# Kernel optimization log

Measured on AMD Instinct MI355X. Metric: run time of the kernel, lower is better.

## Reference

```python
import jax, jax.numpy as jnp
import numpy as np

B = 32
IMG = 512
P = 32            # patch_size (must equal 32 so bounding_box Linear(32,4) type-checks)
G = IMG // P      # 16
N = G * G         # 256 num_patches
PD = P * P * 3    # 3072 patch_dim
D = 512           # project_dim
H = 8             # num_heads
DH = D // H
L = 4             # transformer blocks
HEAD_DIMS = [N * D, 2048, 1024, 512, 64, 32]
EPS = 1e-6


def _mk(key, shape, scale=0.02):
    return (jax.random.normal(key, shape, dtype=jnp.float32) * scale)


def setup_inputs() -> dict:
    key = jax.random.key(0)
    ks = jax.random.split(key, 32)
    inp = {"images": jax.random.normal(ks[0], (B, IMG, IMG, 3), dtype=jnp.float32)}
    # patch encoder
    inp["W_proj"] = _mk(ks[1], (PD, D))
    inp["b_proj"] = jnp.zeros((D,), jnp.float32)
    inp["pos_emb"] = _mk(ks[2], (N, D))
    # stacked transformer block params [L, ...]
    inp["ln1_g"] = jnp.ones((L, D), jnp.float32)
    inp["ln1_b"] = jnp.zeros((L, D), jnp.float32)
    inp["qkv_w"] = _mk(ks[3], (L, 3 * D, D))
    inp["qkv_b"] = jnp.zeros((L, 3 * D), jnp.float32)
    inp["attn_out_w"] = _mk(ks[4], (L, D, D))
    inp["attn_out_b"] = jnp.zeros((L, D), jnp.float32)
    inp["ln2_g"] = jnp.ones((L, D), jnp.float32)
    inp["ln2_b"] = jnp.zeros((L, D), jnp.float32)
    inp["mlp_w1"] = _mk(ks[5], (L, D, 2 * D))
    inp["mlp_b1"] = jnp.zeros((L, 2 * D), jnp.float32)
    inp["mlp_w2"] = _mk(ks[6], (L, 2 * D, D))
    inp["mlp_b2"] = jnp.zeros((L, D), jnp.float32)
    # final LN
    inp["lnf_g"] = jnp.ones((D,), jnp.float32)
    inp["lnf_b"] = jnp.zeros((D,), jnp.float32)
    # MLP head (5 layers) + bbox
    for i in range(5):
        inp[f"hW{i+1}"] = _mk(ks[7 + i], (HEAD_DIMS[i], HEAD_DIMS[i + 1]))
        inp[f"hb{i+1}"] = jnp.zeros((HEAD_DIMS[i + 1],), jnp.float32)
    inp["bbW"] = _mk(ks[20], (32, 4))
    inp["bbb"] = jnp.zeros((4,), jnp.float32)
    return inp


def _ln(x, g, b):
    m = jnp.mean(x, axis=-1, keepdims=True)
    v = jnp.mean((x - m) ** 2, axis=-1, keepdims=True)
    return (x - m) * jax.lax.rsqrt(v + EPS) * g + b


def _patches(images):
    # fused unfold: [B,IMG,IMG,3] -> [B,N,P*P*3], flatten order (ph, pw, c)
    x = images.reshape(B, G, P, G, P, 3)
    x = x.transpose(0, 1, 3, 2, 4, 5)  # [B,G,G,P,P,3]
    return x.reshape(B, N, PD)


def _block(x, ln1_g, ln1_b, qkv_w, qkv_b, out_w, out_b, ln2_g, ln2_b, w1, b1, w2, b2):
    x1 = _ln(x, ln1_g, ln1_b)
    qkv = x1 @ qkv_w.T + qkv_b  # [B,N,3D]
    q, k, v = jnp.split(qkv, 3, axis=-1)
    q = q.reshape(B, N, H, DH).transpose(0, 2, 1, 3)
    k = k.reshape(B, N, H, DH).transpose(0, 2, 1, 3)
    v = v.reshape(B, N, H, DH).transpose(0, 2, 1, 3)
    scores = jnp.einsum("bhqd,bhkd->bhqk", q, k) / jnp.sqrt(jnp.float32(DH))
    attn = jax.nn.softmax(scores, axis=-1)
    o = jnp.einsum("bhqk,bhkd->bhqd", attn, v)
    o = o.transpose(0, 2, 1, 3).reshape(B, N, D)
    attn_out = o @ out_w.T + out_b
    x2 = attn_out + x
    x3 = _ln(x2, ln2_g, ln2_b)
    h = jax.nn.gelu(x3 @ w1 + b1, approximate=False)
    h = jax.nn.gelu(h @ w2 + b2, approximate=False)
    return h + x2


def reference(images, W_proj, b_proj, pos_emb,
              ln1_g, ln1_b, qkv_w, qkv_b, attn_out_w, attn_out_b,
              ln2_g, ln2_b, mlp_w1, mlp_b1, mlp_w2, mlp_b2,
              lnf_g, lnf_b,
              hW1, hb1, hW2, hb2, hW3, hb3, hW4, hb4, hW5, hb5,
              bbW, bbb):
    patches = _patches(images)                       # [B,N,PD]
    x = patches @ W_proj + b_proj + pos_emb          # [B,N,D]
    for i in range(L):
        x = _block(x, ln1_g[i], ln1_b[i], qkv_w[i], qkv_b[i],
                   attn_out_w[i], attn_out_b[i], ln2_g[i], ln2_b[i],
                   mlp_w1[i], mlp_b1[i], mlp_w2[i], mlp_b2[i])
    rep = _ln(x, lnf_g, lnf_b).reshape(B, N * D)
    f = rep
    for (w, b) in [(hW1, hb1), (hW2, hb2), (hW3, hb3), (hW4, hb4), (hW5, hb5)]:
        f = jax.nn.gelu(f @ w + b, approximate=False)
    return f @ bbW + bbb                              # [B,4]
```

## Files before the change

### kernel.cpp

```cpp
#include <hip/hip_runtime.h>
#include <cstdint>
#include <cstddef>

#define DEV __device__ __forceinline__

typedef float f32x4 __attribute__((ext_vector_type(4)));
typedef short s16x8 __attribute__((ext_vector_type(8)));

DEV float gelu_f(float x) { return 0.5f * x * (1.0f + erff(x * 0.70710678118654752f)); }

DEV uint32_t fbits(float x) { return __builtin_bit_cast(uint32_t, x); }

DEV uint16_t bf16_rne(float x) {
    uint32_t u = fbits(x);
    return (uint16_t)((u + 0x7FFFu + ((u >> 16) & 1u)) >> 16);
}

DEV void gload16(const void* g, void* l) {
    __builtin_amdgcn_global_load_lds(
        (const __attribute__((address_space(1))) uint32_t*)g,
        (__attribute__((address_space(3))) uint32_t*)l, 16, 0, 0);
}

template<int BM, int BN, bool BIAS, bool GELU, bool RES, bool POS,
         bool OUTF32, bool OUTB16>
__global__ __launch_bounds__(256)
void mfma_gemm(const uint16_t* __restrict__ Ah, const uint16_t* __restrict__ Bh,
               float* __restrict__ C, uint16_t* __restrict__ Cb,
               const float* __restrict__ bias, const float* __restrict__ res,
               const float* __restrict__ pos, int M, int N, int K)
{
    constexpr int WTM = BM / 2, WTN = BN / 2;
    constexpr int FM = WTM / 16, FN = WTN / 16;
    constexpr int NA = BM / 16, NB = BN / 16;
    constexpr int TI = NA + NB;
    constexpr int TI4 = TI / 4;
    constexpr int HALF = (BM + BN) * 64;
    constexpr int BNP = BN + 4;
    constexpr int SMEM_BYTES = (2 * HALF > BM * BNP * 4) ? 2 * HALF : BM * BNP * 4;

    __shared__ __align__(16) uint8_t smem[SMEM_BYTES];
    constexpr int offB = BM * 64;

    const int tid = threadIdx.x;
    const int w = tid >> 6, l = tid & 63;
    const int wr = w >> 1, wc = w & 1;

    const int gx = gridDim.x;
    const int nwg = gx * gridDim.y;
    const int lin = blockIdx.y * gx + blockIdx.x;
    const int cpx = nwg >> 3;
    const int swz = (lin & 7) * cpx + (lin >> 3);
    const int bxs = swz % gx, bys = swz / gx;
    const int bm0 = bys * BM, bn0 = bxs * BN;
    const size_t sK = (size_t)K * 2;

    const int srow  = l >> 2;
    const int sslot = (l & 3) ^ ((l >> 3) & 3);
    const uint8_t* gsrc[TI4];
    uint32_t loff[TI4];
#pragma unroll
    for (int j = 0; j < TI4; ++j) {
        int f = w * TI4 + j;
        int p = (f < NA) ? 0 : 1;
        int c = p ? (f - NA) : f;
        const uint16_t* base = p ? Bh : Ah;
        int rb = p ? bn0 : bm0;
        gsrc[j] = (const uint8_t*)base + (size_t)(rb + c * 16 + srow) * sK + sslot * 16;
        loff[j] = (uint32_t)((p ? offB : 0) + c * 1024);
    }

    const int lr = l & 15;
    const int sl16 = ((l >> 4) ^ ((lr >> 1) & 3)) * 16;
    const int aofs = (wr * WTM + lr) * 64 + sl16;
    const int bofs = (wc * WTN + lr) * 64 + sl16;

    f32x4 acc[FM][FN];
#pragma unroll
    for (int m = 0; m < FM; ++m)
#pragma unroll
        for (int n = 0; n < FN; ++n) acc[m][n] = (f32x4){0.f, 0.f, 0.f, 0.f};

    {
        const uint8_t* s0 = smem;
#pragma unroll
        for (int j = 0; j < TI4; ++j)
            gload16(gsrc[j], (void*)(s0 + loff[j]));
    }
    asm volatile("s_waitcnt vmcnt(0)" ::: "memory");
    __builtin_amdgcn_s_barrier();

    int cur = 0;
    for (int k0 = 0; k0 < K; k0 += 32) {
        const bool more = (k0 + 32 < K);
        if (more) {
            const size_t kb = (size_t)(k0 + 32) * 2;
            uint8_t* dst = smem + (cur ^ 1) * HALF;
#pragma unroll
            for (int j = 0; j < TI4; ++j)
                gload16(gsrc[j] + kb, dst + loff[j]);
        }
        const uint8_t* sb = smem + cur * HALF;
        s16x8 af[FM], bf[FN];
#pragma unroll
        for (int m = 0; m < FM; ++m)
            af[m] = *(const s16x8*)(sb + aofs + m * 1024);
#pragma unroll
        for (int n = 0; n < FN; ++n)
            bf[n] = *(const s16x8*)(sb + offB + bofs + n * 1024);
#pragma unroll
        for (int m = 0; m < FM; ++m)
#pragma unroll
            for (int n = 0; n < FN; ++n)
                acc[m][n] = __builtin_amdgcn_mfma_f32_16x16x32_bf16(af[m], bf[n], acc[m][n], 0, 0, 0);

        if (more) {
            asm volatile("s_waitcnt vmcnt(0)" ::: "memory");
            __builtin_amdgcn_s_barrier();
        }
        cur ^= 1;
    }

    __syncthreads();
    float* lf = (float*)smem;
    const int r4 = (l >> 4) * 4;
#pragma unroll
    for (int m = 0; m < FM; ++m) {
#pragma unroll
        for (int n = 0; n < FN; ++n) {
            int row = wr * WTM + m * 16 + r4;
            int col = wc * WTN + n * 16 + lr;
#pragma unroll
            for (int r = 0; r < 4; ++r)
                lf[(row + r) * BNP + col] = acc[m][n][r];
        }
    }
    __syncthreads();

    constexpr int C4PR = BN / 4;
    constexpr int RPP  = 256 / C4PR;
    constexpr int NP   = BM / RPP;
    const int rr = tid / C4PR, c4 = tid % C4PR;
    const int nn = bn0 + c4 * 4;

    float4 bv = {0.f, 0.f, 0.f, 0.f};
    if (BIAS) bv = *(const float4*)(bias + nn);

#pragma unroll
    for (int p = 0; p < NP; ++p) {
        int row = p * RPP + rr;
        int mm = bm0 + row;
        float4 v = *(const float4*)&lf[row * BNP + c4 * 4];
        float* vp = &v.x;
        const float* bp = &bv.x;
#pragma unroll
        for (int q = 0; q < 4; ++q) {
            float x = vp[q];
            if (BIAS) x += bp[q];
            if (GELU) x = gelu_f(x);
            vp[q] = x;
        }
        if (RES) {
            float4 rv = *(const float4*)(res + (size_t)mm * N + nn);
            v.x += rv.x; v.y += rv.y; v.z += rv.z; v.w += rv.w;
        }
        if (POS) {
            float4 pv = *(const float4*)(pos + (size_t)(mm & 255) * N + nn);
            v.x += pv.x; v.y += pv.y; v.z += pv.z; v.w += pv.w;
        }
        size_t o = (size_t)mm * N + nn;
        if (OUTF32) *(float4*)(C + o) = v;
        if (OUTB16) {
            ushort4 hh;
            hh.x = bf16_rne(v.x); hh.y = bf16_rne(v.y);
            hh.z = bf16_rne(v.z); hh.w = bf16_rne(v.w);
            *(ushort4*)(Cb + o) = hh;
        }
    }
}

__global__ __launch_bounds__(256)
void mfma_attn(const uint16_t* __restrict__ QKVb, uint16_t* __restrict__ Oh)
{
    __shared__ __align__(16) uint8_t lds[92160];
    uint8_t* Qs = lds;
    uint8_t* Ks = lds + 36864;
    uint8_t* Vt = lds + 46080;
    uint8_t* Ps = lds + 55296;

    const int tid = threadIdx.x;
    const int w = tid >> 6, l = tid & 63;
    const int lr = l & 15, lg = l >> 4;
    const int bh = blockIdx.x;
    const int b = bh >> 3, h = bh & 7;
    const uint16_t* base = QKVb + (size_t)b * 256 * 1536 + h * 64;
    const int q0 = w * 64;

    {
        const uint16_t* qp = base + (size_t)tid * 1536;
#pragma unroll
        for (int s = 0; s < 8; ++s)
            *(s16x8*)(Qs + tid * 144 + s * 16) = *(const s16x8*)(qp + s * 8);
    }

    f32x4 oacc[4][4];
    float lrun[4][4];
#pragma unroll
    for (int m = 0; m < 4; ++m)
#pragma unroll
        for (int n = 0; n < 4; ++n) { oacc[m][n] = (f32x4){0.f,0.f,0.f,0.f}; lrun[m][n] = 0.f; }

    for (int kt = 0; kt < 4; ++kt) {
        __syncthreads();
        {
            int r = tid >> 2, sp = (tid & 3) * 2;
            const uint16_t* kp = base + (size_t)(kt * 64 + r) * 1536 + 512;
#pragma unroll
            for (int ss = 0; ss < 2; ++ss) {
                int s = sp + ss;
                *(s16x8*)(Ks + r * 144 + s * 16) = *(const s16x8*)(kp + s * 8);
            }
        }
        {
            int k = tid & 63, d0 = (tid >> 6) * 16;
            const uint16_t* vp = base + (size_t)(kt * 64 + k) * 1536 + 1024 + d0;
            s16x8 a = *(const s16x8*)(vp);
            s16x8 c = *(const s16x8*)(vp + 8);
#pragma unroll
            for (int i = 0; i < 8; ++i) {
                *(uint16_t*)(Vt + (d0 + i) * 144 + k * 2)     = (uint16_t)a[i];
                *(uint16_t*)(Vt + (d0 + 8 + i) * 144 + k * 2) = (uint16_t)c[i];
            }
        }
        __syncthreads();

        f32x4 sacc[4][4];
#pragma unroll
        for (int m = 0; m < 4; ++m)
#pragma unroll
            for (int n = 0; n < 4; ++n) sacc[m][n] = (f32x4){0.f,0.f,0.f,0.f};
#pragma unroll
        for (int ks = 0; ks < 2; ++ks) {
            s16x8 qf[4], kf[4];
#pragma unroll
            for (int m = 0; m < 4; ++m)
                qf[m] = *(const s16x8*)(Qs + (q0 + m * 16 + lr) * 144 + ks * 64 + lg * 16);
#pragma unroll
            for (int n = 0; n < 4; ++n)
                kf[n] = *(const s16x8*)(Ks + (n * 16 + lr) * 144 + ks * 64 + lg * 16);
#pragma unroll
            for (int m = 0; m < 4; ++m)
#pragma unroll
                for (int n = 0; n < 4; ++n)
                    sacc[m][n] = __builtin_amdgcn_mfma_f32_16x16x32_bf16(qf[m], kf[n], sacc[m][n], 0, 0, 0);
        }

        float dp[4][4];
#pragma unroll
        for (int m = 0; m < 4; ++m)
#pragma unroll
            for (int r = 0; r < 4; ++r) dp[m][r] = 0.f;
#pragma unroll
        for (int m = 0; m < 4; ++m) {
#pragma unroll
            for (int n = 0; n < 4; ++n) {
#pragma unroll
                for (int r = 0; r < 4; ++r) {
                    float e = __expf(sacc[m][n][r] * 0.125f);
                    dp[m][r] += e;
                    int q = q0 + m * 16 + lg * 4 + r;
                    int k = n * 16 + lr;
                    *(uint16_t*)(Ps + q * 144 + k * 2) = bf16_rne(e);
                }
            }
        }
#pragma unroll
        for (int m = 0; m < 4; ++m)
#pragma unroll
            for (int r = 0; r < 4; ++r) {
                float d = dp[m][r];
                d += __shfl_xor(d, 1);
                d += __shfl_xor(d, 2);
                d += __shfl_xor(d, 4);
                d += __shfl_xor(d, 8);
                lrun[m][r] += d;
            }

        asm volatile("s_waitcnt lgkmcnt(0)" ::: "memory");
        __builtin_amdgcn_sched_barrier(0);

#pragma unroll
        for (int ks = 0; ks < 2; ++ks) {
            s16x8 pf[4], vf[4];
#pragma unroll
            for (int m = 0; m < 4; ++m)
                pf[m] = *(const s16x8*)(Ps + (q0 + m * 16 + lr) * 144 + ks * 64 + lg * 16);
#pragma unroll
            for (int n = 0; n < 4; ++n)
                vf[n] = *(const s16x8*)(Vt + (n * 16 + lr) * 144 + ks * 64 + lg * 16);
#pragma unroll
            for (int m = 0; m < 4; ++m)
#pragma unroll
                for (int n = 0; n < 4; ++n)
                    oacc[m][n] = __builtin_amdgcn_mfma_f32_16x16x32_bf16(pf[m], vf[n], oacc[m][n], 0, 0, 0);
        }
    }

    float inv[4][4];
#pragma unroll
    for (int m = 0; m < 4; ++m)
#pragma unroll
        for (int r = 0; r < 4; ++r) inv[m][r] = 1.f / lrun[m][r];

    __syncthreads();
    float* OL = (float*)lds;
#pragma unroll
    for (int m = 0; m < 4; ++m)
#pragma unroll
        for (int n = 0; n < 4; ++n)
#pragma unroll
            for (int r = 0; r < 4; ++r) {
                int q = q0 + m * 16 + lg * 4 + r;
                int d = n * 16 + lr;
                OL[q * 68 + d] = oacc[m][n][r] * inv[m][r];
            }
    __syncthreads();

#pragma unroll
    for (int pass = 0; pass < 16; ++pass) {
        int q = pass * 16 + (tid >> 4);
        int d4 = tid & 15;
        f32x4 v = *(const f32x4*)(OL + q * 68 + d4 * 4);
        ushort4 hh;
        hh.x = bf16_rne(v[0]); hh.y = bf16_rne(v[1]);
        hh.z = bf16_rne(v[2]); hh.w = bf16_rne(v[3]);
        size_t o = (size_t)(b * 256 + q) * 512 + h * 64 + d4 * 4;
        *(ushort4*)(Oh + o) = hh;
    }
}

__global__ __launch_bounds__(256)
void img2planes_kernel(const float* __restrict__ img, uint16_t* __restrict__ Ph)
{
    int idx = blockIdx.x * 256 + threadIdx.x;
    if (idx >= 8192 * 768) return;
    int m = idx / 768, q = idx - (idx / 768) * 768;
    int k = q * 4;
    int bb = m >> 8, n = m & 255;
    int ph = k / 96, rem = k - ph * 96;
    int prow = ((n >> 4) << 5) + ph;
    int pcol0 = (n & 15) << 5;
    const float* s = img + (((size_t)bb * 512 + prow) * 512 + pcol0) * 3 + rem;
    float4 v = *(const float4*)s;
    ushort4 hh;
    hh.x = bf16_rne(v.x); hh.y = bf16_rne(v.y);
    hh.z = bf16_rne(v.z); hh.w = bf16_rne(v.w);
    *(ushort4*)(Ph + (size_t)m * 3072 + k) = hh;
}

__global__ __launch_bounds__(256)
void conv_direct_kernel(const float* __restrict__ src, uint16_t* __restrict__ dh, int total4)
{
    int idx = blockIdx.x * 256 + threadIdx.x;
    if (idx >= total4) return;
    float4 v = *(const float4*)(src + (size_t)idx * 4);
    ushort4 hh;
    hh.x = bf16_rne(v.x); hh.y = bf16_rne(v.y);
    hh.z = bf16_rne(v.z); hh.w = bf16_rne(v.w);
    *(ushort4*)(dh + (size_t)idx * 4) = hh;
}

__global__ __launch_bounds__(256)
void conv_transpose_kernel(const float* __restrict__ src, uint16_t* __restrict__ dh,
                           int K, int N)
{
    __shared__ float t[32][33];
    int k0 = blockIdx.x * 32, n0 = blockIdx.y * 32;
    const float* s = src + (size_t)blockIdx.z * K * N;
    size_t dbase = (size_t)blockIdx.z * N * K;
    int tid = threadIdx.x;
    {
        int kk = tid / 8, n4 = tid % 8;
        float4 v = *(const float4*)(s + (size_t)(k0 + kk) * N + n0 + n4 * 4);
        t[kk][n4 * 4 + 0] = v.x; t[kk][n4 * 4 + 1] = v.y;
        t[kk][n4 * 4 + 2] = v.z; t[kk][n4 * 4 + 3] = v.w;
    }
    __syncthreads();
    int nn = tid / 8, k4 = tid % 8;
    ushort4 hh;
    hh.x = bf16_rne(t[k4 * 4 + 0][nn]);
    hh.y = bf16_rne(t[k4 * 4 + 1][nn]);
    hh.z = bf16_rne(t[k4 * 4 + 2][nn]);
    hh.w = bf16_rne(t[k4 * 4 + 3][nn]);
    *(ushort4*)(dh + dbase + (size_t)(n0 + nn) * K + k0 + k4 * 4) = hh;
}

template<bool PLANES>
__global__ __launch_bounds__(256)
void ln_kernel(const float* __restrict__ X, const float* __restrict__ g,
               const float* __restrict__ b, float* __restrict__ Y,
               uint16_t* __restrict__ Yh, int nrows)
{
    int wave = threadIdx.x >> 6;
    int lane = threadIdx.x & 63;
    int row = blockIdx.x * 4 + wave;
    if (row >= nrows) return;
    const float* x = X + (size_t)row * 512;
    float4 v0 = ((const float4*)x)[lane];
    float4 v1 = ((const float4*)x)[lane + 64];
    float s  = v0.x + v0.y + v0.z + v0.w + v1.x + v1.y + v1.z + v1.w;
    float sq = v0.x*v0.x + v0.y*v0.y + v0.z*v0.z + v0.w*v0.w
             + v1.x*v1.x + v1.y*v1.y + v1.z*v1.z + v1.w*v1.w;
#pragma unroll
    for (int off = 32; off > 0; off >>= 1) {
        s  += __shfl_down(s, off);
        sq += __shfl_down(sq, off);
    }
    s  = __shfl(s, 0);
    sq = __shfl(sq, 0);
    float mean = s * (1.f / 512.f);
    float var  = sq * (1.f / 512.f) - mean * mean;
    float rinv = rsqrtf(var + 1e-6f);
    float4 g0 = ((const float4*)g)[lane], g1 = ((const float4*)g)[lane + 64];
    float4 b0 = ((const float4*)b)[lane], b1 = ((const float4*)b)[lane + 64];
    float4 o0, o1;
    o0.x = (v0.x - mean) * rinv * g0.x + b0.x;
    o0.y = (v0.y - mean) * rinv * g0.y + b0.y;
    o0.z = (v0.z - mean) * rinv * g0.z + b0.z;
    o0.w = (v0.w - mean) * rinv * g0.w + b0.w;
    o1.x = (v1.x - mean) * rinv * g1.x + b1.x;
    o1.y = (v1.y - mean) * rinv * g1.y + b1.y;
    o1.z = (v1.z - mean) * rinv * g1.z + b1.z;
    o1.w = (v1.w - mean) * rinv * g1.w + b1.w;
    if (PLANES) {
        ushort4 hh0, hh1;
        hh0.x = bf16_rne(o0.x); hh0.y = bf16_rne(o0.y);
        hh0.z = bf16_rne(o0.z); hh0.w = bf16_rne(o0.w);
        hh1.x = bf16_rne(o1.x); hh1.y = bf16_rne(o1.y);
        hh1.z = bf16_rne(o1.z); hh1.w = bf16_rne(o1.w);
        size_t base = (size_t)row * 512;
        *(ushort4*)(Yh + base + lane * 4)       = hh0;
        *(ushort4*)(Yh + base + 256 + lane * 4) = hh1;
    } else {
        float* y = Y + (size_t)row * 512;
        ((float4*)y)[lane]      = o0;
        ((float4*)y)[lane + 64] = o1;
    }
}

template<int BM, int BN, int BK, int TM, int TN, bool SPLITK>
__global__ __launch_bounds__(256)
void gemm_kernel(const float* __restrict__ A, const float* __restrict__ B,
                 float* __restrict__ C, int M, int N, int K, int kchunk)
{
    constexpr int TX = BN / TN;
    constexpr int TY = BM / TM;
    static_assert(TX * TY == 256, "bad tile config");
    __shared__ float As[BK][BM + 4];
    __shared__ float Bs[BK][BN + 4];
    const int tid = threadIdx.x;
    const int tx  = tid % TX;
    const int ty  = tid / TX;
    const int bn0 = blockIdx.x * BN;
    const int bm0 = blockIdx.y * BM;
    int kstart = 0, kend = K;
    if (SPLITK) { kstart = blockIdx.z * kchunk; kend = kstart + kchunk; }
    float acc[TM][TN];
#pragma unroll
    for (int i = 0; i < TM; ++i)
#pragma unroll
        for (int j = 0; j < TN; ++j) acc[i][j] = 0.f;
    for (int k0 = kstart; k0 < kend; k0 += BK) {
        __syncthreads();
        constexpr int AV = BM * BK / 4 / 256;
#pragma unroll
        for (int r = 0; r < AV; ++r) {
            int idx = tid + r * 256;
            int k4 = idx % (BK / 4);
            int mm = idx / (BK / 4);
            float4 v = *(const float4*)(A + (size_t)(bm0 + mm) * K + k0 + k4 * 4);
            As[k4 * 4 + 0][mm] = v.x;
            As[k4 * 4 + 1][mm] = v.y;
            As[k4 * 4 + 2][mm] = v.z;
            As[k4 * 4 + 3][mm] = v.w;
        }
        constexpr int BV = BK * BN / 4 / 256;
#pragma unroll
        for (int r = 0; r < BV; ++r) {
            int idx = tid + r * 256;
            int n4 = idx % (BN / 4);
            int kk = idx / (BN / 4);
            float4 v = *(const float4*)(B + (size_t)(k0 + kk) * N + bn0 + n4 * 4);
            *(float4*)&Bs[kk][n4 * 4] = v;
        }
        __syncthreads();
#pragma unroll
        for (int kk = 0; kk < BK; ++kk) {
            float a[TM], b[TN];
#pragma unroll
            for (int i = 0; i < TM; i += 4)
                *(float4*)&a[i] = *(const float4*)&As[kk][ty * TM + i];
#pragma unroll
            for (int j = 0; j < TN; j += 4)
                *(float4*)&b[j] = *(const float4*)&Bs[kk][tx * TN + j];
#pragma unroll
            for (int i = 0; i < TM; ++i)
#pragma unroll
                for (int j = 0; j < TN; ++j)
                    acc[i][j] = fmaf(a[i], b[j], acc[i][j]);
        }
    }
    float* Cb = C;
    if (SPLITK) Cb += (size_t)blockIdx.z * M * N;
#pragma unroll
    for (int i = 0; i < TM; ++i) {
        int m = bm0 + ty * TM + i;
#pragma unroll
        for (int j = 0; j < TN; j += 4) {
            int n = bn0 + tx * TN + j;
            float4 v;
            v.x = acc[i][j + 0]; v.y = acc[i][j + 1];
            v.z = acc[i][j + 2]; v.w = acc[i][j + 3];
            *(float4*)(Cb + (size_t)m * N + n) = v;
        }
    }
}

__global__ __launch_bounds__(256)
void skinny_gemm_kernel(const float* __restrict__ A, const float* __restrict__ B,
                        float* __restrict__ P, int M, int N, int K, int kchunk)
{
    __shared__ float As[32][36];
    const int tid = threadIdx.x;
    const int tx  = tid & 63;
    const int ty  = tid >> 6;
    const int bn0 = blockIdx.x * 64;
    const int kstart = blockIdx.y * kchunk;
    const int kend   = kstart + kchunk;
    float acc[8];
#pragma unroll
    for (int i = 0; i < 8; ++i) acc[i] = 0.f;
    for (int k0 = kstart; k0 < kend; k0 += 32) {
        __syncthreads();
        {
            int row = tid >> 3;
            int k4  = tid & 7;
            float4 v = *(const float4*)(A + (size_t)row * K + k0 + k4 * 4);
            *(float4*)&As[row][k4 * 4] = v;
        }
        __syncthreads();
#pragma unroll 8
        for (int kk = 0; kk < 32; ++kk) {
            float b = B[(size_t)(k0 + kk) * N + bn0 + tx];
#pragma unroll
            for (int i = 0; i < 8; ++i)
                acc[i] = fmaf(As[ty * 8 + i][kk], b, acc[i]);
        }
    }
    float* Pb = P + (size_t)blockIdx.y * M * N;
#pragma unroll
    for (int i = 0; i < 8; ++i)
        Pb[(size_t)(ty * 8 + i) * N + bn0 + tx] = acc[i];
}

__global__ __launch_bounds__(256)
void reduce_gelu_kernel(const float* __restrict__ P, const float* __restrict__ bias,
                        float* __restrict__ Y, int total, int chunks, int N)
{
    int idx = blockIdx.x * 256 + threadIdx.x;
    if (idx >= total) return;
    float s = 0.f;
    for (int c = 0; c < chunks; ++c) s += P[(size_t)c * total + idx];
    s += bias[idx % N];
    Y[idx] = gelu_f(s);
}

template<bool GELU>
__global__ __launch_bounds__(256)
void small_gemm_kernel(const float* __restrict__ A, const float* __restrict__ B,
                       const float* __restrict__ bias, float* __restrict__ C,
                       int M, int N, int K)
{
    int idx = blockIdx.x * 256 + threadIdx.x;
    if (idx >= M * N) return;
    int m = idx / N, n = idx % N;
    const float* a = A + (size_t)m * K;
    float s = 0.f;
    for (int k = 0; k < K; ++k) s = fmaf(a[k], B[(size_t)k * N + n], s);
    s += bias[n];
    if (GELU) s = gelu_f(s);
    C[idx] = s;
}

extern "C" void kernel_launch(void* const* d_in, const int* in_sizes, int n_in,
                              void* d_out, int out_size, void* d_ws, size_t ws_size,
                              hipStream_t stream)
{
    const float* images     = (const float*)d_in[0];
    const float* W_proj     = (const float*)d_in[1];
    const float* b_proj     = (const float*)d_in[2];
    const float* pos_emb    = (const float*)d_in[3];
    const float* ln1_g      = (const float*)d_in[4];
    const float* ln1_b      = (const float*)d_in[5];
    const float* qkv_w      = (const float*)d_in[6];
    const float* qkv_b      = (const float*)d_in[7];
    const float* attn_out_w = (const float*)d_in[8];
    const float* attn_out_b = (const float*)d_in[9];
    const float* ln2_g      = (const float*)d_in[10];
    const float* ln2_b      = (const float*)d_in[11];
    const float* mlp_w1     = (const float*)d_in[12];
    const float* mlp_b1     = (const float*)d_in[13];
    const float* mlp_w2     = (const float*)d_in[14];
    const float* mlp_b2     = (const float*)d_in[15];
    const float* lnf_g      = (const float*)d_in[16];
    const float* lnf_b      = (const float*)d_in[17];
    const float* hW1 = (const float*)d_in[18];
    const float* hb1 = (const float*)d_in[19];
    const float* hW2 = (const float*)d_in[20];
    const float* hb2 = (const float*)d_in[21];
    const float* hW3 = (const float*)d_in[22];
    const float* hb3 = (const float*)d_in[23];
    const float* hW4 = (const float*)d_in[24];
    const float* hb4 = (const float*)d_in[25];
    const float* hW5 = (const float*)d_in[26];
    const float* hb5 = (const float*)d_in[27];
    const float* bbW = (const float*)d_in[28];
    const float* bbb = (const float*)d_in[29];

    uint8_t* wsb = (uint8_t*)d_ws;
    size_t off = 0;
    auto alloc = [&](size_t bytes) { uint8_t* p = wsb + off; off += (bytes + 255) & ~(size_t)255; return p; };
    float*    X    = (float*)alloc(8192ull * 512 * 4);
    uint16_t* QKVb = (uint16_t*)alloc(8192ull * 1536 * 2);
    float*    T    = (float*)alloc(8192ull * 512 * 4);
    uint16_t* Xh   = (uint16_t*)alloc(8192ull * 512 * 2);
    uint16_t* Ohp  = (uint16_t*)alloc(8192ull * 512 * 2);
    uint16_t* Hh   = (uint16_t*)alloc(8192ull * 1024 * 2);
    uint16_t* Ph   = (uint16_t*)alloc(8192ull * 3072 * 2);
    uint16_t* WqH  = (uint16_t*)alloc(4ull * 1536 * 512 * 2);
    uint16_t* WaH  = (uint16_t*)alloc(4ull * 512 * 512 * 2);
    uint16_t* WpH  = (uint16_t*)alloc(512ull * 3072 * 2);
    uint16_t* W1H  = (uint16_t*)alloc(4ull * 1024 * 512 * 2);
    uint16_t* W2H  = (uint16_t*)alloc(4ull * 512 * 1024 * 2);
    float*    F1p  = (float*)alloc(128ull * 65536 * 4);
    float*    F1   = (float*)alloc(65536ull * 4);
    float*    P2   = (float*)alloc(64ull * 32768 * 4);
    float*    F2   = (float*)alloc(32768ull * 4);
    float*    P3   = (float*)alloc(32ull * 16384 * 4);
    float*    F3   = (float*)alloc(16384ull * 4);
    float*    P4   = (float*)alloc(16ull * 2048 * 4);
    float*    F4   = (float*)alloc(2048ull * 4);
    float*    F5   = (float*)alloc(1024ull * 4);

    dim3 blk(256);

    img2planes_kernel<<<(8192 * 768 + 255) / 256, blk, 0, stream>>>(images, Ph);
    conv_direct_kernel<<<(4 * 1536 * 512 / 4 + 255) / 256, blk, 0, stream>>>(qkv_w, WqH, 4 * 1536 * 512 / 4);
    conv_direct_kernel<<<(4 * 512 * 512 / 4 + 255) / 256, blk, 0, stream>>>(attn_out_w, WaH, 4 * 512 * 512 / 4);
    conv_transpose_kernel<<<dim3(3072 / 32, 512 / 32, 1), blk, 0, stream>>>(W_proj, WpH, 3072, 512);
    conv_transpose_kernel<<<dim3(512 / 32, 1024 / 32, 4), blk, 0, stream>>>(mlp_w1, W1H, 512, 1024);
    conv_transpose_kernel<<<dim3(1024 / 32, 512 / 32, 4), blk, 0, stream>>>(mlp_w2, W2H, 1024, 512);

    mfma_gemm<64, 128, true, false, false, true, true, false>
        <<<dim3(512 / 128, 8192 / 64), blk, 0, stream>>>(
            Ph, WpH, X, nullptr, b_proj, nullptr, pos_emb, 8192, 512, 3072);

    for (int l = 0; l < 4; ++l) {
        ln_kernel<true><<<2048, blk, 0, stream>>>(X, ln1_g + l * 512, ln1_b + l * 512,
                                                  nullptr, Xh, 8192);
        mfma_gemm<128, 128, true, false, false, false, false, true>
            <<<dim3(1536 / 128, 8192 / 128), blk, 0, stream>>>(
                Xh, WqH + (size_t)l * 1536 * 512, nullptr, QKVb,
                qkv_b + l * 1536, nullptr, nullptr, 8192, 1536, 512);
        mfma_attn<<<256, blk, 0, stream>>>(QKVb, Ohp);
        mfma_gemm<64, 128, true, false, true, false, true, false>
            <<<dim3(512 / 128, 8192 / 64), blk, 0, stream>>>(
                Ohp, WaH + (size_t)l * 512 * 512, X, nullptr,
                attn_out_b + l * 512, X, nullptr, 8192, 512, 512);
        ln_kernel<true><<<2048, blk, 0, stream>>>(X, ln2_g + l * 512, ln2_b + l * 512,
                                                  nullptr, Xh, 8192);
        mfma_gemm<128, 128, true, true, false, false, false, true>
            <<<dim3(1024 / 128, 8192 / 128), blk, 0, stream>>>(
                Xh, W1H + (size_t)l * 1024 * 512, nullptr, Hh,
                mlp_b1 + l * 1024, nullptr, nullptr, 8192, 1024, 512);
        mfma_gemm<64, 128, true, true, true, false, true, false>
            <<<dim3(512 / 128, 8192 / 64), blk, 0, stream>>>(
                Hh, W2H + (size_t)l * 512 * 1024, X, nullptr,
                mlp_b2 + l * 512, X, nullptr, 8192, 512, 1024);
    }

    ln_kernel<false><<<2048, blk, 0, stream>>>(X, lnf_g, lnf_b, T, nullptr, 8192);

    gemm_kernel<32, 128, 32, 4, 4, true>
        <<<dim3(2048 / 128, 1, 128), blk, 0, stream>>>(
            T, hW1, F1p, 32, 2048, 131072, 131072 / 128);
    reduce_gelu_kernel<<<(65536 + 255) / 256, blk, 0, stream>>>(F1p, hb1, F1, 65536, 128, 2048);

    skinny_gemm_kernel<<<dim3(1024 / 64, 2048 / 32), blk, 0, stream>>>(F1, hW2, P2, 32, 1024, 2048, 32);
    reduce_gelu_kernel<<<(32768 + 255) / 256, blk, 0, stream>>>(P2, hb2, F2, 32768, 64, 1024);

    skinny_gemm_kernel<<<dim3(512 / 64, 1024 / 32), blk, 0, stream>>>(F2, hW3, P3, 32, 512, 1024, 32);
    reduce_gelu_kernel<<<(16384 + 255) / 256, blk, 0, stream>>>(P3, hb3, F3, 16384, 32, 512);

    skinny_gemm_kernel<<<dim3(64 / 64, 512 / 32), blk, 0, stream>>>(F3, hW4, P4, 32, 64, 512, 32);
    reduce_gelu_kernel<<<(2048 + 255) / 256, blk, 0, stream>>>(P4, hb4, F4, 2048, 16, 64);

    small_gemm_kernel<true><<<(32 * 32 + 255) / 256, blk, 0, stream>>>(F4, hW5, hb5, F5, 32, 32, 64);
    small_gemm_kernel<false><<<1, blk, 0, stream>>>(F5, bbW, bbb, (float*)d_out, 32, 4, 32);
}
```

Measured before the change: 1.060 ms.

## Shrink LDS footprint in GEMM epilogue and attention to raise occupancy

After: 1.125 ms. +6.2%, slower.

```diff
diff --git a/kernel.cpp b/kernel.cpp
--- a/kernel.cpp
+++ b/kernel.cpp
@@ -37,9 +37,11 @@
     constexpr int TI4 = TI / 4;
     constexpr int HALF = (BM + BN) * 64;
     constexpr int BNP = BN + 4;
-    constexpr int SMEM_BYTES = (2 * HALF > BM * BNP * 4) ? 2 * HALF : BM * BNP * 4;
-
-    __shared__ __align__(16) uint8_t smem[SMEM_BYTES];
+    constexpr int CR  = 32;
+    constexpr int NCH = BM / CR;
+    static_assert(CR * BNP * 4 <= 2 * HALF, "chunk must fit LDS");
+
+    __shared__ __align__(16) uint8_t smem[2 * HALF];
     constexpr int offB = BM * 64;
 
     const int tid = threadIdx.x;
@@ -121,25 +123,11 @@
         cur ^= 1;
     }
 
-    __syncthreads();
     float* lf = (float*)smem;
     const int r4 = (l >> 4) * 4;
-#pragma unroll
-    for (int m = 0; m < FM; ++m) {
-#pragma unroll
-        for (int n = 0; n < FN; ++n) {
-            int row = wr * WTM + m * 16 + r4;
-            int col = wc * WTN + n * 16 + lr;
-#pragma unroll
-            for (int r = 0; r < 4; ++r)
-                lf[(row + r) * BNP + col] = acc[m][n][r];
-        }
-    }
-    __syncthreads();
 
     constexpr int C4PR = BN / 4;
     constexpr int RPP  = 256 / C4PR;
-    constexpr int NP   = BM / RPP;
     const int rr = tid / C4PR, c4 = tid % C4PR;
     const int nn = bn0 + c4 * 4;
 
@@ -147,34 +135,55 @@
     if (BIAS) bv = *(const float4*)(bias + nn);
 
 #pragma unroll
-    for (int p = 0; p < NP; ++p) {
-        int row = p * RPP + rr;
-        int mm = bm0 + row;
-        float4 v = *(const float4*)&lf[row * BNP + c4 * 4];
-        float* vp = &v.x;
-        const float* bp = &bv.x;
-#pragma unroll
-        for (int q = 0; q < 4; ++q) {
-            float x = vp[q];
-            if (BIAS) x += bp[q];
-            if (GELU) x = gelu_f(x);
-            vp[q] = x;
-        }
-        if (RES) {
-            float4 rv = *(const float4*)(res + (size_t)mm * N + nn);
-            v.x += rv.x; v.y += rv.y; v.z += rv.z; v.w += rv.w;
-        }
-        if (POS) {
-            float4 pv = *(const float4*)(pos + (size_t)(mm & 255) * N + nn);
-            v.x += pv.x; v.y += pv.y; v.z += pv.z; v.w += pv.w;
-        }
-        size_t o = (size_t)mm * N + nn;
-        if (OUTF32) *(float4*)(C + o) = v;
-        if (OUTB16) {
-            ushort4 hh;
-            hh.x = bf16_rne(v.x); hh.y = bf16_rne(v.y);
-            hh.z = bf16_rne(v.z); hh.w = bf16_rne(v.w);
-            *(ushort4*)(Cb + o) = hh;
+    for (int c = 0; c < NCH; ++c) {
+        __syncthreads();
+        if (wr == (c * CR) / WTM) {
+            const int mlo = ((c * CR) % WTM) / 16;
+#pragma unroll
+            for (int mi = 0; mi < CR / 16; ++mi) {
+                int m = mlo + mi;
+#pragma unroll
+                for (int n = 0; n < FN; ++n) {
+                    int col = wc * WTN + n * 16 + lr;
+#pragma unroll
+                    for (int r = 0; r < 4; ++r) {
+                        int lrow = mi * 16 + r4 + r;
+                        lf[lrow * BNP + col] = acc[m][n][r];
+                    }
+                }
+            }
+        }
+        __syncthreads();
+#pragma unroll
+        for (int p = 0; p < CR / RPP; ++p) {
+            int row = p * RPP + rr;
+            int mm = bm0 + c * CR + row;
+            float4 v = *(const float4*)&lf[row * BNP + c4 * 4];
+            float* vp = &v.x;
+            const float* bp = &bv.x;
+#pragma unroll
+            for (int q = 0; q < 4; ++q) {
+                float x = vp[q];
+                if (BIAS) x += bp[q];
+                if (GELU) x = gelu_f(x);
+                vp[q] = x;
+            }
+            if (RES) {
+                float4 rv = *(const float4*)(res + (size_t)mm * N + nn);
+                v.x += rv.x; v.y += rv.y; v.z += rv.z; v.w += rv.w;
+            }
+            if (POS) {
+                float4 pv = *(const float4*)(pos + (size_t)(mm & 255) * N + nn);
+                v.x += pv.x; v.y += pv.y; v.z += pv.z; v.w += pv.w;
+            }
+            size_t o = (size_t)mm * N + nn;
+            if (OUTF32) *(float4*)(C + o) = v;
+            if (OUTB16) {
+                ushort4 hh;
+                hh.x = bf16_rne(v.x); hh.y = bf16_rne(v.y);
+                hh.z = bf16_rne(v.z); hh.w = bf16_rne(v.w);
+                *(ushort4*)(Cb + o) = hh;
+            }
         }
     }
 }
@@ -182,11 +191,10 @@
 __global__ __launch_bounds__(256)
 void mfma_attn(const uint16_t* __restrict__ QKVb, uint16_t* __restrict__ Oh)
 {
-    __shared__ __align__(16) uint8_t lds[92160];
-    uint8_t* Qs = lds;
-    uint8_t* Ks = lds + 36864;
-    uint8_t* Vt = lds + 46080;
-    uint8_t* Ps = lds + 55296;
+    __shared__ __align__(16) uint8_t lds[55296];
+    uint8_t* Ks = lds;
+    uint8_t* Vt = lds + 9216;
+    uint8_t* Ps = lds + 18432;
 
     const int tid = threadIdx.x;
     const int w = tid >> 6, l = tid & 63;
@@ -196,12 +204,12 @@
     const uint16_t* base = QKVb + (size_t)b * 256 * 1536 + h * 64;
     const int q0 = w * 64;
 
-    {
-        const uint16_t* qp = base + (size_t)tid * 1536;
-#pragma unroll
-        for (int s = 0; s < 8; ++s)
-            *(s16x8*)(Qs + tid * 144 + s * 16) = *(const s16x8*)(qp + s * 8);
-    }
+    s16x8 qreg[2][4];
+#pragma unroll
+    for (int ks = 0; ks < 2; ++ks)
+#pragma unroll
+        for (int m = 0; m < 4; ++m)
+            qreg[ks][m] = *(const s16x8*)(base + (size_t)(q0 + m * 16 + lr) * 1536 + ks * 32 + lg * 8);
 
     f32x4 oacc[4][4];
     float lrun[4][4];
@@ -241,10 +249,7 @@
             for (int n = 0; n < 4; ++n) sacc[m][n] = (f32x4){0.f,0.f,0.f,0.f};
 #pragma unroll
         for (int ks = 0; ks < 2; ++ks) {
-            s16x8 qf[4], kf[4];
-#pragma unroll
-            for (int m = 0; m < 4; ++m)
-                qf[m] = *(const s16x8*)(Qs + (q0 + m * 16 + lr) * 144 + ks * 64 + lg * 16);
+            s16x8 kf[4];
 #pragma unroll
             for (int n = 0; n < 4; ++n)
                 kf[n] = *(const s16x8*)(Ks + (n * 16 + lr) * 144 + ks * 64 + lg * 16);
@@ -252,7 +257,7 @@
             for (int m = 0; m < 4; ++m)
 #pragma unroll
                 for (int n = 0; n < 4; ++n)
-                    sacc[m][n] = __builtin_amdgcn_mfma_f32_16x16x32_bf16(qf[m], kf[n], sacc[m][n], 0, 0, 0);
+                    sacc[m][n] = __builtin_amdgcn_mfma_f32_16x16x32_bf16(qreg[ks][m], kf[n], sacc[m][n], 0, 0, 0);
         }
 
         float dp[4][4];
@@ -312,30 +317,36 @@
 #pragma unroll
         for (int r = 0; r < 4; ++r) inv[m][r] = 1.f / lrun[m][r];
 
-    __syncthreads();
     float* OL = (float*)lds;
 #pragma unroll
-    for (int m = 0; m < 4; ++m)
-#pragma unroll
-        for (int n = 0; n < 4; ++n)
-#pragma unroll
-            for (int r = 0; r < 4; ++r) {
-                int q = q0 + m * 16 + lg * 4 + r;
-                int d = n * 16 + lr;
-                OL[q * 68 + d] = oacc[m][n][r] * inv[m][r];
-            }
-    __syncthreads();
-
-#pragma unroll
-    for (int pass = 0; pass < 16; ++pass) {
-        int q = pass * 16 + (tid >> 4);
-        int d4 = tid & 15;
-        f32x4 v = *(const f32x4*)(OL + q * 68 + d4 * 4);
-        ushort4 hh;
-        hh.x = bf16_rne(v[0]); hh.y = bf16_rne(v[1]);
-        hh.z = bf16_rne(v[2]); hh.w = bf16_rne(v[3]);
-        size_t o = (size_t)(b * 256 + q) * 512 + h * 64 + d4 * 4;
-        *(ushort4*)(Oh + o) = hh;
+    for (int c = 0; c < 2; ++c) {
+        __syncthreads();
+        if ((w >> 1) == c) {
+            const int lq0 = q0 - c * 128;
+#pragma unroll
+            for (int m = 0; m < 4; ++m)
+#pragma unroll
+                for (int n = 0; n < 4; ++n)
+#pragma unroll
+                    for (int r = 0; r < 4; ++r) {
+                        int lq = lq0 + m * 16 + lg * 4 + r;
+                        int d = n * 16 + lr;
+                        OL[lq * 68 + d] = oacc[m][n][r] * inv[m][r];
+                    }
+        }
+        __syncthreads();
+#pragma unroll
+        for (int p = 0; p < 8; ++p) {
+            int lq = p * 16 + (tid >> 4);
+            int q = c * 128 + lq;
+            int d4 = tid & 15;
+            f32x4 v = *(const f32x4*)(OL + lq * 68 + d4 * 4);
+            ushort4 hh;
+            hh.x = bf16_rne(v[0]); hh.y = bf16_rne(v[1]);
+            hh.z = bf16_rne(v[2]); hh.w = bf16_rne(v[3]);
+            size_t o = (size_t)(b * 256 + q) * 512 + h * 64 + d4 * 4;
+            *(ushort4*)(Oh + o) = hh;
+        }
     }
 }
 
@@ -661,8 +672,8 @@
     conv_transpose_kernel<<<dim3(512 / 32, 1024 / 32, 4), blk, 0, stream>>>(mlp_w1, W1H, 512, 1024);
     conv_transpose_kernel<<<dim3(1024 / 32, 512 / 32, 4), blk, 0, stream>>>(mlp_w2, W2H, 1024, 512);
 
-    mfma_gemm<64, 128, true, false, false, true, true, false>
-        <<<dim3(512 / 128, 8192 / 64), blk, 0, stream>>>(
+    mfma_gemm<128, 128, true, false, false, true, true, false>
+        <<<dim3(512 / 128, 8192 / 128), blk, 0, stream>>>(
             Ph, WpH, X, nullptr, b_proj, nullptr, pos_emb, 8192, 512, 3072);
 
     for (int l = 0; l < 4; ++l) {
@@ -673,8 +684,8 @@
                 Xh, WqH + (size_t)l * 1536 * 512, nullptr, QKVb,
                 qkv_b + l * 1536, nullptr, nullptr, 8192, 1536, 512);
         mfma_attn<<<256, blk, 0, stream>>>(QKVb, Ohp);
-        mfma_gemm<64, 128, true, false, true, false, true, false>
-            <<<dim3(512 / 128, 8192 / 64), blk, 0, stream>>>(
+        mfma_gemm<128, 128, true, false, true, false, true, false>
+            <<<dim3(512 / 128, 8192 / 128), blk, 0, stream>>>(
                 Ohp, WaH + (size_t)l * 512 * 512, X, nullptr,
                 attn_out_b + l * 512, X, nullptr, 8192, 512, 512);
         ln_kernel<true><<<2048, blk, 0, stream>>>(X, ln2_g + l * 512, ln2_b + l * 512,
@@ -683,8 +694,8 @@
             <<<dim3(1024 / 128, 8192 / 128), blk, 0, stream>>>(
                 Xh, W1H + (size_t)l * 1024 * 512, nullptr, Hh,
                 mlp_b1 + l * 1024, nullptr, nullptr, 8192, 1024, 512);
-        mfma_gemm<64, 128, true, true, true, false, true, false>
-            <<<dim3(512 / 128, 8192 / 64), blk, 0, stream>>>(
+        mfma_gemm<128, 128, true, true, true, false, true, false>
+            <<<dim3(512 / 128, 8192 / 128), blk, 0, stream>>>(
                 Hh, W2H + (size_t)l * 512 * 1024, X, nullptr,
                 mlp_b2 + l * 512, X, nullptr, 8192, 512, 1024);
     }
```
